# Performance work log

Measured on AMD Instinct MI355X. Metric: run time of the kernel, lower is better.

## Reference

```python
import jax, jax.numpy as jnp
import numpy as np

DIM = 96          # dense volume side (N_VOX / 2**(n_layer-scale-1) with scale=2)
C = 24            # ch_in[scale]
FEAT_INIT = 0.0   # not direct_substitute


def _scatter_channel(coords, values, ch, default, dtype=jnp.float32):
    """sparse_to_dense_channel: dense[x,y,z] = values; OOB coords are dropped."""
    vol = jnp.full((DIM, DIM, DIM, ch), default, dtype=dtype)
    return vol.at[coords[:, 0], coords[:, 1], coords[:, 2]].set(values, mode='drop')


def _mask_coords(coords, valid):
    # Replace invalid rows with an out-of-bounds index so scatter mode='drop' skips them
    return jnp.where(valid[:, None], coords, DIM)


def setup_inputs() -> dict:
    key = jax.random.key(0)
    ks = jax.random.split(key, 9)
    return {
        'current_coords': jax.random.randint(ks[0], (150000, 3), 0, DIM, dtype=jnp.int32),
        'current_values': jax.random.normal(ks[1], (150000, C), dtype=jnp.float32),
        'global_coords_raw': jax.random.randint(ks[2], (200000, 3), 0, 160, dtype=jnp.int32),
        'global_values': jax.random.normal(ks[3], (200000, C), dtype=jnp.float32),
        'coords_target_global': jax.random.randint(ks[4], (100000, 3), 0, DIM, dtype=jnp.int32),
        'tsdf_target': jax.random.uniform(ks[5], (100000,), dtype=jnp.float32) * 2.0 - 1.0,
        'global_coords_target_raw': jax.random.randint(ks[6], (120000, 3), 0, 160, dtype=jnp.int32),
        'global_tsdf_target': jax.random.uniform(ks[7], (120000, 1), dtype=jnp.float32) * 2.0 - 1.0,
        'relative_origin': jax.random.randint(ks[8], (3,), 0, 32, dtype=jnp.int32),
    }


def reference(current_coords, current_values, global_coords_raw, global_values,
              coords_target_global, tsdf_target, global_coords_target_raw,
              global_tsdf_target, relative_origin):
    # --- shift global coords into current fragment frame, compute FBV mask ---
    gc = global_coords_raw - relative_origin[None, :]
    valid = jnp.all((gc >= 0) & (gc < DIM), axis=-1)                     # (M,)

    # --- FUSION.FULL is False: keep only global voxels present in current sparse set ---
    valid_volume = jnp.zeros((DIM, DIM, DIM), dtype=jnp.int32)
    valid_volume = valid_volume.at[current_coords[:, 0], current_coords[:, 1],
                                   current_coords[:, 2]].set(1, mode='drop')
    gcc = jnp.clip(gc, 0, DIM - 1)
    occ = valid_volume[gcc[:, 0], gcc[:, 1], gcc[:, 2]]
    valid = valid & (occ != 0)

    # --- dense scatters (sparse_to_dense_channel) ---
    global_volume = _scatter_channel(_mask_coords(gc, valid), global_values, C, FEAT_INIT)
    current_volume = _scatter_channel(current_coords, current_values, C, FEAT_INIT)

    # updated_coords = current_coords (FULL is False branch)
    updated_coords = current_coords

    gtc = global_coords_target_raw - relative_origin[None, :]
    valid_target = jnp.all((gtc >= 0) & (gtc < DIM), axis=-1)            # (Mt,)
    coords_target = jnp.concatenate([_mask_coords(gtc, valid_target), coords_target_global], axis=0)
    tsdf_all = jnp.concatenate([global_tsdf_target, tsdf_target[:, None]], axis=0)
    target_volume = _scatter_channel(coords_target, tsdf_all, 1, 1.0)

    return updated_coords, current_volume, global_volume, target_volume, valid, valid_target
```

## Files before the change

kernel.cpp:

```cpp
#include <hip/hip_runtime.h>

#define DIMV 96
#define NCH 24
constexpr int VOX = DIMV * DIMV * DIMV;
constexpr int N_CUR = 150000;
constexpr int N_GLB = 200000;
constexpr int N_TGT_LOC = 100000;
constexpr int N_TGT_GLB = 120000;

constexpr size_t OFF_COORDS = 0;
constexpr size_t OFF_CURVOL = 450000;
constexpr size_t OFF_GLBVOL = OFF_CURVOL + (size_t)VOX * NCH;
constexpr size_t OFF_TGTVOL = OFF_GLBVOL + (size_t)VOX * NCH;
constexpr size_t OFF_VALID  = OFF_TGTVOL + (size_t)VOX;
constexpr size_t OFF_VALIDT = OFF_VALID + N_GLB;

typedef float v4f __attribute__((ext_vector_type(4)));
typedef int   v4i __attribute__((ext_vector_type(4)));

constexpr int N_COORD4 = (N_CUR * 3) / 4;
constexpr int NV4_WS   = (3 * VOX) / 4;

__device__ __forceinline__ int voxel_of(int x, int y, int z) {
    return (x * DIMV + y) * DIMV + z;
}

__global__ void __launch_bounds__(256) k_init(int* __restrict__ ws,
                                              const int* __restrict__ cur_coords,
                                              float* __restrict__ coords_out) {
    int i = blockIdx.x * blockDim.x + threadIdx.x;
    if (i < NV4_WS) {
        v4i m = {-1, -1, -1, -1};
        *((v4i*)ws + i) = m;
    } else if (i < NV4_WS + N_COORD4) {
        int j = i - NV4_WS;
        v4i c = *(const v4i*)(cur_coords + 4 * j);
        v4f f = {(float)c.x, (float)c.y, (float)c.z, (float)c.w};
        *((v4f*)coords_out + j) = f;
    }
}

__global__ void k_points(const int* __restrict__ cur_coords,
                         const int* __restrict__ tgt_coords_g,
                         const int* __restrict__ tgt_coords_l,
                         const int* __restrict__ glb_coords,
                         const int* __restrict__ origin,
                         int* __restrict__ w_cur,
                         int* __restrict__ w_tgt,
                         int* __restrict__ w_glb,
                         float* __restrict__ validt_out) {
    int i = blockIdx.x * blockDim.x + threadIdx.x;
    if (i < N_CUR) {
        int x = cur_coords[3 * i], y = cur_coords[3 * i + 1], z = cur_coords[3 * i + 2];
        if ((unsigned)x < DIMV && (unsigned)y < DIMV && (unsigned)z < DIMV)
            atomicMax(&w_cur[voxel_of(x, y, z)], i);
    } else if (i < N_CUR + N_TGT_GLB) {
        int j = i - N_CUR;
        int x = tgt_coords_g[3 * j]     - origin[0];
        int y = tgt_coords_g[3 * j + 1] - origin[1];
        int z = tgt_coords_g[3 * j + 2] - origin[2];
        bool inb = (unsigned)x < DIMV && (unsigned)y < DIMV && (unsigned)z < DIMV;
        validt_out[j] = inb ? 1.0f : 0.0f;
        if (inb) atomicMax(&w_tgt[voxel_of(x, y, z)], j);
    } else if (i < N_CUR + N_TGT_GLB + N_TGT_LOC) {
        int j = i - N_CUR - N_TGT_GLB;
        int x = tgt_coords_l[3 * j], y = tgt_coords_l[3 * j + 1], z = tgt_coords_l[3 * j + 2];
        if ((unsigned)x < DIMV && (unsigned)y < DIMV && (unsigned)z < DIMV)
            atomicMax(&w_tgt[voxel_of(x, y, z)], j + N_TGT_GLB);
    } else if (i < N_CUR + N_TGT_GLB + N_TGT_LOC + N_GLB) {
        int j = i - N_CUR - N_TGT_GLB - N_TGT_LOC;
        int x = glb_coords[3 * j]     - origin[0];
        int y = glb_coords[3 * j + 1] - origin[1];
        int z = glb_coords[3 * j + 2] - origin[2];
        if ((unsigned)x < DIMV && (unsigned)y < DIMV && (unsigned)z < DIMV)
            atomicMax(&w_glb[voxel_of(x, y, z)], j);
    }
}

constexpr int SEG_B = N_GLB * 6;
constexpr int SEG_A = N_CUR * 6;
constexpr int SEG_T = N_TGT_GLB + N_TGT_LOC;
constexpr int SEG_F = VOX * 6;
constexpr int FILL_TOTAL = SEG_B + SEG_A + SEG_T + SEG_F;

__global__ void __launch_bounds__(256) k_fill_all(
                           const int* __restrict__ w_cur,
                           const int* __restrict__ w_glb,
                           const int* __restrict__ w_tgt,
                           const int* __restrict__ cur_coords,
                           const int* __restrict__ glb_coords,
                           const int* __restrict__ tgt_coords_g,
                           const int* __restrict__ tgt_coords_l,
                           const int* __restrict__ origin,
                           const float* __restrict__ cur_values,
                           const float* __restrict__ glb_values,
                           const float* __restrict__ glb_tsdf,
                           const float* __restrict__ loc_tsdf,
                           float* __restrict__ cur_out,
                           float* __restrict__ glb_out,
                           float* __restrict__ tgt_out,
                           float* __restrict__ valid_out) {
    int i = blockIdx.x * blockDim.x + threadIdx.x;
    if (i < SEG_B) {
        int p = i / 6, q = i - p * 6;
        int x = glb_coords[3 * p]     - origin[0];
        int y = glb_coords[3 * p + 1] - origin[1];
        int z = glb_coords[3 * p + 2] - origin[2];
        bool inb = (unsigned)x < DIMV && (unsigned)y < DIMV && (unsigned)z < DIMV;
        int cx = min(max(x, 0), DIMV - 1);
        int cy = min(max(y, 0), DIMV - 1);
        int cz = min(max(z, 0), DIMV - 1);
        int v = voxel_of(cx, cy, cz);
        bool occ = w_cur[v] >= 0;
        if (q == 0) valid_out[p] = (inb && occ) ? 1.0f : 0.0f;
        if (inb && occ && w_glb[v] == p)
            *(v4f*)(glb_out + (size_t)v * NCH + q * 4) =
                *(const v4f*)(glb_values + (size_t)p * NCH + q * 4);
    } else if (i < SEG_B + SEG_A) {
        int t = i - SEG_B;
        int p = t / 6, q = t - p * 6;
        int x = cur_coords[3 * p], y = cur_coords[3 * p + 1], z = cur_coords[3 * p + 2];
        if ((unsigned)x < DIMV && (unsigned)y < DIMV && (unsigned)z < DIMV) {
            int v = voxel_of(x, y, z);
            if (w_cur[v] == p)
                *(v4f*)(cur_out + (size_t)v * NCH + q * 4) =
                    *(const v4f*)(cur_values + (size_t)p * NCH + q * 4);
        }
    } else if (i < SEG_B + SEG_A + SEG_T) {
        int j = i - SEG_B - SEG_A;
        if (j < N_TGT_GLB) {
            int x = tgt_coords_g[3 * j]     - origin[0];
            int y = tgt_coords_g[3 * j + 1] - origin[1];
            int z = tgt_coords_g[3 * j + 2] - origin[2];
            if ((unsigned)x < DIMV && (unsigned)y < DIMV && (unsigned)z < DIMV) {
                int v = voxel_of(x, y, z);
                if (w_tgt[v] == j) tgt_out[v] = glb_tsdf[j];
            }
        } else {
            int jj = j - N_TGT_GLB;
            int x = tgt_coords_l[3 * jj], y = tgt_coords_l[3 * jj + 1], z = tgt_coords_l[3 * jj + 2];
            if ((unsigned)x < DIMV && (unsigned)y < DIMV && (unsigned)z < DIMV) {
                int v = voxel_of(x, y, z);
                if (w_tgt[v] == j + N_TGT_GLB) tgt_out[v] = loc_tsdf[jj];
            }
        }
    } else if (i < FILL_TOTAL) {
        int c = i - SEG_B - SEG_A - SEG_T;
        int v = c / 6, q = c - v * 6;
        const v4f zero = (v4f){0.f, 0.f, 0.f, 0.f};

        int wc = w_cur[v];
        if (wc < 0)
            *(v4f*)(cur_out + (size_t)v * NCH + q * 4) = zero;

        int wg = w_glb[v];
        if (wc < 0 || wg < 0)
            *(v4f*)(glb_out + (size_t)v * NCH + q * 4) = zero;

        if (q == 0 && w_tgt[v] < 0)
            tgt_out[v] = 1.0f;
    }
}

extern "C" void kernel_launch(void* const* d_in, const int* in_sizes, int n_in,
                              void* d_out, int out_size, void* d_ws, size_t ws_size,
                              hipStream_t stream) {
    const int*   cur_coords   = (const int*)d_in[0];
    const float* cur_values   = (const float*)d_in[1];
    const int*   glb_coords   = (const int*)d_in[2];
    const float* glb_values   = (const float*)d_in[3];
    const int*   tgt_coords_l = (const int*)d_in[4];
    const float* tgt_tsdf_l   = (const float*)d_in[5];
    const int*   tgt_coords_g = (const int*)d_in[6];
    const float* tgt_tsdf_g   = (const float*)d_in[7];
    const int*   rel_origin   = (const int*)d_in[8];

    float* out = (float*)d_out;
    int* w_cur = (int*)d_ws;
    int* w_glb = w_cur + VOX;
    int* w_tgt = w_glb + VOX;

    const int T = 256;
    auto blocks = [](int n) { return (n + 255) / 256; };

    k_init<<<blocks(NV4_WS + N_COORD4), T, 0, stream>>>(
        (int*)d_ws, cur_coords, out + OFF_COORDS);

    k_points<<<blocks(N_CUR + N_TGT_GLB + N_TGT_LOC + N_GLB), T, 0, stream>>>(
        cur_coords, tgt_coords_g, tgt_coords_l, glb_coords, rel_origin,
        w_cur, w_tgt, w_glb, out + OFF_VALIDT);

    k_fill_all<<<blocks(FILL_TOTAL), T, 0, stream>>>(
        w_cur, w_glb, w_tgt, cur_coords, glb_coords, tgt_coords_g, tgt_coords_l,
        rel_origin, cur_values, glb_values, tgt_tsdf_g, tgt_tsdf_l,
        out + OFF_CURVOL, out + OFF_GLBVOL, out + OFF_TGTVOL, out + OFF_VALID);
}
```

Measured before the change: 62.85 us.

## Fuse unconditional background fill into scatter kernel; fix local target winner check

The background pass that read the three winner maps per voxel and conditionally wrote zeros or ones is removed. The point-scatter kernel now also blindly zeroes both feature volumes and writes 1.0 across the target volume, running alongside the atomic index scatter. The payload kernel then overwrites the winning voxels. This drops the per-voxel winner-map reads and index division, at the cost of also writing the occupied voxels twice. It also corrects the local-target winner comparison, which previously added the global-target offset a second time.

```diff
diff --git a/kernel.cpp b/kernel.cpp
--- a/kernel.cpp
+++ b/kernel.cpp
@@ -40,7 +40,13 @@
     }
 }
 
-__global__ void k_points(const int* __restrict__ cur_coords,
+constexpr int P_TOTAL = N_CUR + N_TGT_GLB + N_TGT_LOC + N_GLB;
+constexpr int Z4 = (VOX * NCH * 2) / 4;
+constexpr int T4 = VOX / 4;
+constexpr int WORK_TOTAL = P_TOTAL + Z4 + T4;
+
+__global__ void __launch_bounds__(256) k_work(
+                         const int* __restrict__ cur_coords,
                          const int* __restrict__ tgt_coords_g,
                          const int* __restrict__ tgt_coords_l,
                          const int* __restrict__ glb_coords,
@@ -48,7 +54,9 @@
                          int* __restrict__ w_cur,
                          int* __restrict__ w_tgt,
                          int* __restrict__ w_glb,
-                         float* __restrict__ validt_out) {
+                         float* __restrict__ validt_out,
+                         float* __restrict__ vol_base,
+                         float* __restrict__ tgt_out) {
     int i = blockIdx.x * blockDim.x + threadIdx.x;
     if (i < N_CUR) {
         int x = cur_coords[3 * i], y = cur_coords[3 * i + 1], z = cur_coords[3 * i + 2];
@@ -67,23 +75,28 @@
         int x = tgt_coords_l[3 * j], y = tgt_coords_l[3 * j + 1], z = tgt_coords_l[3 * j + 2];
         if ((unsigned)x < DIMV && (unsigned)y < DIMV && (unsigned)z < DIMV)
             atomicMax(&w_tgt[voxel_of(x, y, z)], j + N_TGT_GLB);
-    } else if (i < N_CUR + N_TGT_GLB + N_TGT_LOC + N_GLB) {
+    } else if (i < P_TOTAL) {
         int j = i - N_CUR - N_TGT_GLB - N_TGT_LOC;
         int x = glb_coords[3 * j]     - origin[0];
         int y = glb_coords[3 * j + 1] - origin[1];
         int z = glb_coords[3 * j + 2] - origin[2];
         if ((unsigned)x < DIMV && (unsigned)y < DIMV && (unsigned)z < DIMV)
             atomicMax(&w_glb[voxel_of(x, y, z)], j);
+    } else if (i < P_TOTAL + Z4) {
+        int j = i - P_TOTAL;
+        *((v4f*)vol_base + j) = (v4f){0.f, 0.f, 0.f, 0.f};
+    } else if (i < WORK_TOTAL) {
+        int j = i - P_TOTAL - Z4;
+        *((v4f*)tgt_out + j) = (v4f){1.f, 1.f, 1.f, 1.f};
     }
 }
 
 constexpr int SEG_B = N_GLB * 6;
 constexpr int SEG_A = N_CUR * 6;
 constexpr int SEG_T = N_TGT_GLB + N_TGT_LOC;
-constexpr int SEG_F = VOX * 6;
-constexpr int FILL_TOTAL = SEG_B + SEG_A + SEG_T + SEG_F;
+constexpr int PAYLOAD_TOTAL = SEG_B + SEG_A + SEG_T;
 
-__global__ void __launch_bounds__(256) k_fill_all(
+__global__ void __launch_bounds__(256) k_payload(
                            const int* __restrict__ w_cur,
                            const int* __restrict__ w_glb,
                            const int* __restrict__ w_tgt,
@@ -126,7 +139,7 @@
                 *(v4f*)(cur_out + (size_t)v * NCH + q * 4) =
                     *(const v4f*)(cur_values + (size_t)p * NCH + q * 4);
         }
-    } else if (i < SEG_B + SEG_A + SEG_T) {
+    } else if (i < PAYLOAD_TOTAL) {
         int j = i - SEG_B - SEG_A;
         if (j < N_TGT_GLB) {
             int x = tgt_coords_g[3 * j]     - origin[0];
@@ -141,24 +154,9 @@
             int x = tgt_coords_l[3 * jj], y = tgt_coords_l[3 * jj + 1], z = tgt_coords_l[3 * jj + 2];
             if ((unsigned)x < DIMV && (unsigned)y < DIMV && (unsigned)z < DIMV) {
                 int v = voxel_of(x, y, z);
-                if (w_tgt[v] == j + N_TGT_GLB) tgt_out[v] = loc_tsdf[jj];
+                if (w_tgt[v] == j) tgt_out[v] = loc_tsdf[jj];
             }
         }
-    } else if (i < FILL_TOTAL) {
-        int c = i - SEG_B - SEG_A - SEG_T;
-        int v = c / 6, q = c - v * 6;
-        const v4f zero = (v4f){0.f, 0.f, 0.f, 0.f};
-
-        int wc = w_cur[v];
-        if (wc < 0)
-            *(v4f*)(cur_out + (size_t)v * NCH + q * 4) = zero;
-
-        int wg = w_glb[v];
-        if (wc < 0 || wg < 0)
-            *(v4f*)(glb_out + (size_t)v * NCH + q * 4) = zero;
-
-        if (q == 0 && w_tgt[v] < 0)
-            tgt_out[v] = 1.0f;
     }
 }
 
@@ -186,11 +184,12 @@
     k_init<<<blocks(NV4_WS + N_COORD4), T, 0, stream>>>(
         (int*)d_ws, cur_coords, out + OFF_COORDS);
 
-    k_points<<<blocks(N_CUR + N_TGT_GLB + N_TGT_LOC + N_GLB), T, 0, stream>>>(
+    k_work<<<blocks(WORK_TOTAL), T, 0, stream>>>(
         cur_coords, tgt_coords_g, tgt_coords_l, glb_coords, rel_origin,
-        w_cur, w_tgt, w_glb, out + OFF_VALIDT);
+        w_cur, w_tgt, w_glb, out + OFF_VALIDT,
+        out + OFF_CURVOL, out + OFF_TGTVOL);
 
-    k_fill_all<<<blocks(FILL_TOTAL), T, 0, stream>>>(
+    k_payload<<<blocks(PAYLOAD_TOTAL), T, 0, stream>>>(
         w_cur, w_glb, w_tgt, cur_coords, glb_coords, tgt_coords_g, tgt_coords_l,
         rel_origin, cur_values, glb_values, tgt_tsdf_g, tgt_tsdf_l,
         out + OFF_CURVOL, out + OFF_GLBVOL, out + OFF_TGTVOL, out + OFF_VALID);
```

After: 61.57 us. -2.0%, faster.
